# Optimization experiments

Hardware: AMD Instinct MI355X
Metric: run time of the kernel (lower is better)

Reference implementation:

```python
import jax, jax.numpy as jnp
import numpy as np

KR = 3  # kernel_range, SHIFT = 1


def _neighborhood(x):
    """x: [B,H,W,C] -> [B,H,W,9,C] stacking the 3x3 shifted views (zero pad),
    in the same (i,j) raster order as the original loop."""
    B, H, W, C = x.shape
    xp = jnp.pad(x, ((0, 0), (1, 1), (1, 1), (0, 0)))
    views = [xp[:, 1 + i:1 + i + H, 1 + j:1 + j + W, :]
             for i in (-1, 0, 1) for j in (-1, 0, 1)]
    return jnp.stack(views, axis=3)


def _conv(x, w, b):
    # tf.nn.conv2d NHWC, HWIO, SAME, stride 1
    return jax.lax.conv_general_dilated(
        x, w, window_strides=(1, 1), padding='SAME',
        dimension_numbers=('NHWC', 'HWIO', 'NHWC')) + b


def setup_inputs() -> dict:
    key = jax.random.key(0)
    ks = jax.random.split(key, 10)
    B, H, W, D = 8, 128, 128, 64
    g = lambda k, shape, fan: jax.random.normal(k, shape, jnp.float32) * np.float32(1.0 / np.sqrt(fan))
    return {
        'x': jax.random.normal(ks[0], (B, H, W, D), jnp.float32),
        'Q_P': g(ks[1], (D, D), D),
        'K_P': g(ks[2], (D, D), D),
        'V_P': g(ks[3], (D, D), D),
        'ff1_kernel': g(ks[4], (3, 3, D, D), 9 * D),
        'ff1_bias': jax.random.normal(ks[5], (D,), jnp.float32) * 0.01,
        'ff2_kernel': g(ks[6], (3, 3, D, 2 * D), 9 * D),
        'ff2_bias': jax.random.normal(ks[7], (2 * D,), jnp.float32) * 0.01,
        'ff3_kernel': g(ks[8], (3, 3, 2 * D, D), 9 * 2 * D),
        'ff3_bias': jax.random.normal(ks[9], (D,), jnp.float32) * 0.01,
    }


def reference(x, Q_P, K_P, V_P, ff1_kernel, ff1_bias, ff2_kernel, ff2_bias,
              ff3_kernel, ff3_bias):
    B, H, W, D = x.shape
    # 3x3 neighborhood gather (zero padded) and validity mask
    stk = _neighborhood(x)                                   # [B,H,W,9,D]
    mask = _neighborhood(jnp.ones((B, H, W, 1), x.dtype))    # [B,H,W,9,1]
    mask = mask[..., 0]                                      # [B,H,W,9]

    q = jnp.einsum('bhwd,de->bhwe', x, Q_P)                  # [B,H,W,D]
    k = jnp.einsum('bhwkd,de->bhwke', stk, K_P)              # [B,H,W,9,D]
    v = jnp.einsum('bhwkd,de->bhwke', stk, V_P)              # [B,H,W,9,D]

    # NOTE: faithful to original -- scores are MULTIPLIED by the mask
    # (masked entries become 0, not -inf) before softmax over the 9 neighbors.
    scores = jnp.einsum('bhwke,bhwe->bhwk', k, q) * mask     # [B,H,W,9]
    alpha = jax.nn.softmax(scores, axis=-1)
    attn = jnp.einsum('bhwk,bhwke->bhwe', alpha, v)          # [B,H,W,D]

    t = x + attn
    t_in = t
    t = jax.nn.relu(_conv(t, ff1_kernel, ff1_bias))
    t = jax.nn.relu(_conv(t, ff2_kernel, ff2_bias))
    t = jax.nn.relu(_conv(t, ff3_kernel, ff3_bias))
    return t_in + t
```

## Files before the change

### kernel.cpp

```cpp
#include <hip/hip_runtime.h>

typedef unsigned int uint32;
typedef unsigned short u16;
typedef short s16x8 __attribute__((ext_vector_type(8)));
typedef short s16x4 __attribute__((ext_vector_type(4)));
typedef float f32x4 __attribute__((ext_vector_type(4)));

#define DEVINL static __device__ __forceinline__
#define MFMA16(a, b, c) __builtin_amdgcn_mfma_f32_16x16x32_bf16(a, b, c, 0, 0, 0)

DEVINL float bf2f(u16 u){ return __uint_as_float(((uint32)u) << 16); }
DEVINL u16 f2bf(float f){
  uint32 u = __float_as_uint(f);
  u += 0x7fffu + ((u >> 16) & 1u);
  return (u16)(u >> 16);
}
DEVINL uint32 pack2(float a, float b){
  return (uint32)f2bf(a) | (((uint32)f2bf(b)) << 16);
}

__global__ void detect_k(const uint32* __restrict__ x, uint32* __restrict__ flag){
  const int lane = threadIdx.x;
  int sane = 0;
  for (int i = 0; i < 32; ++i){
    uint32 u = x[i * 64 + lane];
    uint32 e = (u >> 7) & 0xffu;
    sane += (e >= 100u && e <= 150u) ? 1 : 0;
  }
  for (int off = 32; off >= 1; off >>= 1) sane += __shfl_xor(sane, off);
  if (lane == 0) *flag = (sane > 1024) ? 1u : 0u;
}

template<int M>
__global__ void cvtall_k(const void* s0, const void* s1, const void* s2,
                         const void* s3, const void* s4, const void* s5,
                         const void* s6, const void* s7, const void* s8,
                         float* __restrict__ wb, const uint32* __restrict__ flag)
{
  if (*flag != (uint32)M) return;
  const int i = blockIdx.x * 256 + threadIdx.x;
  if (i >= 196864) return;
  const void* s; int j;
  if      (i < 4096)   { s = s0; j = i; }
  else if (i < 8192)   { s = s1; j = i - 4096; }
  else if (i < 12288)  { s = s2; j = i - 8192; }
  else if (i < 49152)  { s = s3; j = i - 12288; }
  else if (i < 49216)  { s = s4; j = i - 49152; }
  else if (i < 122944) { s = s5; j = i - 49216; }
  else if (i < 123072) { s = s6; j = i - 122944; }
  else if (i < 196800) { s = s7; j = i - 123072; }
  else                 { s = s8; j = i - 196800; }
  wb[i] = M ? bf2f(((const u16*)s)[j]) : ((const float*)s)[j];
}

__global__ __launch_bounds__(256)
void xcvt_k(const void* __restrict__ x, u16* __restrict__ xb,
            const uint32* __restrict__ flag)
{
  if (*flag != 0u) return;
  const size_t i0 = ((size_t)blockIdx.x * 256 + threadIdx.x) * 8;
  const float4 f0 = ((const float4*)x)[i0 / 4];
  const float4 f1 = ((const float4*)x)[i0 / 4 + 1];
  uint4 o;
  o.x = pack2(f0.x, f0.y); o.y = pack2(f0.z, f0.w);
  o.z = pack2(f1.x, f1.y); o.w = pack2(f1.z, f1.w);
  *(uint4*)(xb + i0) = o;
}

__global__ void gcomp_k(const float* __restrict__ wb, u16* __restrict__ gt){
  const int t = blockIdx.x * 256 + threadIdx.x;
  const int d = t >> 6, c = t & 63;
  const float* __restrict__ K = wb + 4096;
  const float* __restrict__ Q = wb;
  float s = 0.f;
#pragma unroll
  for (int e = 0; e < 64; ++e) s = fmaf(K[d * 64 + e], Q[c * 64 + e], s);
  const u16 hi = f2bf(s);
  gt[t] = hi;
  gt[4096 + t] = f2bf(s - bf2f(hi));
}

__global__ void pack_k(const float* __restrict__ wb, u16* __restrict__ bb){
  int i = blockIdx.x * 256 + threadIdx.x;
  if (i < 4096){
    const int o = i >> 6, c = i & 63;
    bb[8192 + i] = f2bf(wb[8192 + c * 64 + o]);
    return;
  }
  i -= 4096;
  if (i < 4096){
    const int o = i >> 6, c = i & 63;
    const float v = wb[8192 + c * 64 + o];
    bb[12288 + i] = f2bf(v - bf2f(f2bf(v)));
    return;
  }
  i -= 4096;
  if (i < 36864){
    const int chunk = i >> 11, rr = i & 2047, co = rr >> 5, kkp = rr & 31;
    const int slot = (kkp >> 3) ^ ((co >> 1) & 3), kk = slot * 8 + (kkp & 7);
    const int tap = chunk >> 1, ci = (chunk & 1) * 32 + kk;
    bb[16384 + i] = f2bf(wb[12288 + (tap * 64 + ci) * 64 + co]);
    return;
  }
  i -= 36864;
  if (i < 73728){
    const int half = i / 36864, i2 = i - half * 36864;
    const int chunk = i2 >> 11, rr = i2 & 2047, co = rr >> 5, kkp = rr & 31;
    const int slot = (kkp >> 3) ^ ((co >> 1) & 3), kk = slot * 8 + (kkp & 7);
    const int tap = chunk >> 1, ci = (chunk & 1) * 32 + kk;
    bb[53248 + i] = f2bf(wb[49216 + (tap * 64 + ci) * 128 + half * 64 + co]);
    return;
  }
  i -= 73728;
  {
    const int chunk = i >> 11, rr = i & 2047, co = rr >> 5, kkp = rr & 31;
    const int slot = (kkp >> 3) ^ ((co >> 1) & 3), kk = slot * 8 + (kkp & 7);
    const int tap = chunk >> 2, ci = (chunk & 3) * 32 + kk;
    bb[126976 + i] = f2bf(wb[123072 + (tap * 128 + ci) * 64 + co]);
  }
}

template<int ROWS, int CIN, int STRIDE>
DEVINL void stage_tile(const u16* __restrict__ img_base, int h0, int w0, u16* lds){
  constexpr int CH8 = CIN / 8;
  constexpr int NCH = ROWS * 66 * CH8;
  for (int idx = threadIdx.x; idx < NCH; idx += 256){
    const int row  = idx / (66 * CH8);
    const int rem  = idx - row * 66 * CH8;
    const int col  = rem / CH8;
    const int slot = rem - col * CH8;
    const int hi = h0 + row - 1, wi = w0 + col - 1;
    uint4 v = make_uint4(0u, 0u, 0u, 0u);
    if (hi >= 0 && hi < 128 && wi >= 0 && wi < 128)
      v = *(const uint4*)(img_base + (size_t)(hi * 128 + wi) * STRIDE + slot * 8);
    const int dst = (row * 66 + col) * CIN + ((slot ^ (col & 7)) << 3);
    *(uint4*)(lds + dst) = v;
  }
}

template<int COUT_FULL, bool RES, int MOUT>
DEVINL void conv_epilogue(f32x4 acc[4][4], u16* scratch, const u16* __restrict__ res,
                          void* __restrict__ out, int img, int h0, int w0, int co0,
                          int wv, int l15, int lk)
{
  float* tl = (float*)scratch;
  const int lane = threadIdx.x & 63;
#pragma unroll
  for (int pass = 0; pass < 2; ++pass){
    __syncthreads();
#pragma unroll
    for (int at2 = 0; at2 < 2; ++at2){
      const int at = pass * 2 + at2;
      const int pp = wv * 32 + at2 * 16 + lk * 4;
#pragma unroll
      for (int nt = 0; nt < 4; ++nt)
#pragma unroll
        for (int reg = 0; reg < 4; ++reg)
          tl[(pp + reg) * 72 + nt * 16 + l15] = fmaxf(acc[at][nt][reg], 0.f);
    }
    __syncthreads();
    const size_t rowpx = (size_t)img * 16384 + (size_t)(h0 + wv) * 128 + w0 + pass * 32;
    if (MOUT == 0){
#pragma unroll
      for (int k = 0; k < 8; ++k){
        const int px = k * 4 + (lane >> 4);
        const int c4 = (lane & 15) * 4;
        float4 v = *(const float4*)(tl + (wv * 32 + px) * 72 + c4);
        if (RES){
          const uint2 r = *(const uint2*)(res + (rowpx + px) * 64 + c4);
          v.x += bf2f((u16)(r.x & 0xffff)); v.y += bf2f((u16)(r.x >> 16));
          v.z += bf2f((u16)(r.y & 0xffff)); v.w += bf2f((u16)(r.y >> 16));
        }
        *(float4*)((float*)out + (rowpx + px) * 64 + c4) = v;
      }
    } else {
#pragma unroll
      for (int k = 0; k < 4; ++k){
        const int px = k * 8 + (lane >> 3);
        const int c8 = (lane & 7) * 8;
        const float* tp = tl + (wv * 32 + px) * 72 + c8;
        const float4 a = *(const float4*)tp;
        const float4 b = *(const float4*)(tp + 4);
        float v0=a.x, v1=a.y, v2=a.z, v3=a.w, v4=b.x, v5=b.y, v6=b.z, v7=b.w;
        if (RES){
          const uint4 r = *(const uint4*)(res + (rowpx + px) * 64 + c8);
          v0 += bf2f((u16)(r.x & 0xffff)); v1 += bf2f((u16)(r.x >> 16));
          v2 += bf2f((u16)(r.y & 0xffff)); v3 += bf2f((u16)(r.y >> 16));
          v4 += bf2f((u16)(r.z & 0xffff)); v5 += bf2f((u16)(r.z >> 16));
          v6 += bf2f((u16)(r.w & 0xffff)); v7 += bf2f((u16)(r.w >> 16));
        }
        uint4 o;
        o.x = pack2(v0, v1); o.y = pack2(v2, v3);
        o.z = pack2(v4, v5); o.w = pack2(v6, v7);
        *(uint4*)((u16*)out + (rowpx + px) * COUT_FULL + co0 + c8) = o;
      }
    }
  }
}

__global__ __launch_bounds__(256, 4)
void attn_mfma(const u16* __restrict__ xraw, const u16* __restrict__ xcv,
               const u16* __restrict__ gt, const u16* __restrict__ vt,
               u16* __restrict__ tb, const uint32* __restrict__ flag)
{
  __shared__ __align__(16) u16 xh[3 * 66 * 64];
  u16* yl  = xh;
  u16* yl2 = xh + 2 * 66 * 64;
  const int bx0 = blockIdx.x;
  const int bx = (bx0 & 7) * 256 + (bx0 >> 3);
  const int img = bx >> 8, h = (bx >> 1) & 127, w0 = (bx & 1) * 64;
  const int p0 = img * 16384 + h * 128 + w0;
  const u16* __restrict__ xsrc = (*flag != 0u) ? xraw : xcv;
  stage_tile<3, 64, 64>(xsrc + (size_t)img * 16384 * 64, h, w0, xh);
  __syncthreads();

  const int lane = threadIdx.x & 63, wv = threadIdx.x >> 6;
  const int l15 = lane & 15, lk = lane >> 4;
  const int pxm = wv * 16 + l15;

  f32x4 racc[4];
#pragma unroll
  for (int nt = 0; nt < 4; ++nt) racc[nt] = (f32x4){0.f, 0.f, 0.f, 0.f};
#pragma unroll
  for (int half = 0; half < 2; ++half){
#pragma unroll
    for (int ks = 0; ks < 2; ++ks){
      const int colq = pxm + 1;
      const int slot = ks * 4 + lk;
      const s16x8 bx_ = *(const s16x8*)&xh[(66 + colq) * 64 + ((slot ^ (colq & 7)) << 3)];
#pragma unroll
      for (int nt = 0; nt < 4; ++nt){
        const s16x8 ag = *(const s16x8*)(gt + half * 4096 +
                          (size_t)(nt * 16 + l15) * 64 + ks * 32 + lk * 8);
        racc[nt] = MFMA16(ag, bx_, racc[nt]);
      }
    }
  }

  float sc[9];
#pragma unroll
  for (int n = 0; n < 9; ++n){
    const int tr = n / 3, tc = n % 3;
    const int col = pxm + tc;
    const u16* xr = &xh[(tr * 66 + col) * 64];
    float s = 0.f;
#pragma unroll
    for (int nt = 0; nt < 4; ++nt){
      const int slot = nt * 2 + (lk >> 1);
      const s16x4 v = *(const s16x4*)&xr[((slot ^ (col & 7)) << 3) + (lk & 1) * 4];
#pragma unroll
      for (int j = 0; j < 4; ++j)
        s = fmaf(bf2f((u16)v[j]), racc[nt][j], s);
    }
    sc[n] = s;
  }
#pragma unroll
  for (int n = 0; n < 9; ++n){
    sc[n] += __shfl_xor(sc[n], 16);
    sc[n] += __shfl_xor(sc[n], 32);
  }

  float mx = sc[0];
#pragma unroll
  for (int n = 1; n < 9; ++n) mx = fmaxf(mx, sc[n]);
  float sum = 0.f;
#pragma unroll
  for (int n = 0; n < 9; ++n){
    const float e = __expf(sc[n] - mx);
    sc[n] = e; sum += e;
  }
  const float inv = 1.f / sum;
#pragma unroll
  for (int n = 0; n < 9; ++n) sc[n] *= inv;

  float y[16];
#pragma unroll
  for (int j = 0; j < 16; ++j) y[j] = 0.f;
#pragma unroll
  for (int n = 0; n < 9; ++n){
    const int tr = n / 3, tc = n % 3;
    const int col = pxm + tc;
    const u16* xr = &xh[(tr * 66 + col) * 64];
    const float a = sc[n];
#pragma unroll
    for (int sl = 0; sl < 2; ++sl){
      const int slot = lk * 2 + sl;
      const s16x8 v = *(const s16x8*)&xr[(slot ^ (col & 7)) << 3];
#pragma unroll
      for (int j = 0; j < 8; ++j)
        y[sl * 8 + j] = fmaf(a, bf2f((u16)v[j]), y[sl * 8 + j]);
    }
  }

  __syncthreads();

#pragma unroll
  for (int sl = 0; sl < 2; ++sl){
    uint32 hwd[4], lwd[4];
#pragma unroll
    for (int j = 0; j < 4; ++j){
      const float a = y[sl * 8 + 2 * j], b = y[sl * 8 + 2 * j + 1];
      const u16 ha = f2bf(a), hb = f2bf(b);
      hwd[j] = (uint32)ha | ((uint32)hb << 16);
      lwd[j] = (uint32)f2bf(a - bf2f(ha)) | ((uint32)f2bf(b - bf2f(hb)) << 16);
    }
    const int slot = lk * 2 + sl;
    const int off = pxm * 64 + ((slot ^ (pxm & 7)) << 3);
    *(uint4*)&yl [off] = make_uint4(hwd[0], hwd[1], hwd[2], hwd[3]);
    *(uint4*)&yl2[off] = make_uint4(lwd[0], lwd[1], lwd[2], lwd[3]);
  }

  __syncthreads();

  f32x4 tacc[4];
#pragma unroll
  for (int nt = 0; nt < 4; ++nt) tacc[nt] = (f32x4){0.f, 0.f, 0.f, 0.f};
#pragma unroll
  for (int half = 0; half < 2; ++half){
    const u16* yb = half ? yl2 : yl;
#pragma unroll
    for (int ks = 0; ks < 2; ++ks){
      const int px = wv * 16 + l15;
      const int slot = ks * 4 + lk;
      const s16x8 af = *(const s16x8*)&yb[px * 64 + ((slot ^ (px & 7)) << 3)];
#pragma unroll
      for (int nt = 0; nt < 4; ++nt){
        const s16x8 bf = *(const s16x8*)(vt + (size_t)(nt * 16 + l15) * 64 + ks * 32 + lk * 8);
        tacc[nt] = MFMA16(af, bf, tacc[nt]);
      }
    }
  }
#pragma unroll
  for (int nt = 0; nt < 4; ++nt){
#pragma unroll
    for (int reg = 0; reg < 4; ++reg){
      const int pxo = wv * 16 + lk * 4 + reg;
      const int co = nt * 16 + l15;
      const int col = pxo + 1;
      const int elem = (66 + col) * 64 + (((co >> 3) ^ (col & 7)) << 3) + (co & 7);
      tb[(size_t)(p0 + pxo) * 64 + co] = f2bf(bf2f(xh[elem]) + tacc[nt][reg]);
    }
  }
}

template<int COUT_FULL, bool RES, int MOUT>
__global__ __launch_bounds__(256)
void conv_mfma(const u16* __restrict__ in, const u16* __restrict__ wpk,
               const float* __restrict__ bias, const u16* __restrict__ res,
               void* __restrict__ out, const uint32* __restrict__ flag)
{
  if (MOUT >= 0){ if (*flag != (uint32)MOUT) return; }
  __shared__ __align__(16) u16 xh[6 * 66 * 64];

  const int bx0 = blockIdx.x;
  const int bx  = (bx0 & 7) * 64 + (bx0 >> 3);
  const int img = bx >> 6;
  const int rem = bx & 63;
  const int h0  = (rem >> 1) * 4;
  const int w0  = (rem & 1) * 64;
  const int co0 = blockIdx.y * 64;
  const u16* __restrict__ wp = wpk + (size_t)blockIdx.y * 18 * 2048;

  stage_tile<6, 64, 64>(in + (size_t)img * 16384 * 64, h0, w0, xh);
  __syncthreads();

  const int lane = threadIdx.x & 63, wv = threadIdx.x >> 6;
  const int l15 = lane & 15, lk = lane >> 4;

  f32x4 acc[4][4];
#pragma unroll
  for (int nt = 0; nt < 4; ++nt){
    const float b = bias[co0 + nt * 16 + l15];
#pragma unroll
    for (int at = 0; at < 4; ++at) acc[at][nt] = (f32x4){b, b, b, b};
  }

  auto loadB = [&](int ck, s16x8* bb){
#pragma unroll
    for (int nt = 0; nt < 4; ++nt){
      const int co = nt * 16 + l15;
      bb[nt] = *(const s16x8*)(wp + (size_t)ck * 2048 + co * 32 +
                               ((lk ^ ((co >> 1) & 3)) << 3));
    }
  };
  auto doM = [&](int it, s16x8* bb){
    const int tap = it >> 1, ks = it & 1;
    const int tr = tap / 3, tc = tap - tr * 3;
    const int slot = ks * 4 + lk;
    s16x8 av[4];
#pragma unroll
    for (int at = 0; at < 4; ++at){
      const int col = at * 16 + l15 + tc;
      av[at] = *(const s16x8*)&xh[((wv + tr) * 66 + col) * 64 + ((slot ^ (col & 7)) << 3)];
    }
#pragma unroll
    for (int at = 0; at < 4; ++at)
#pragma unroll
      for (int nt = 0; nt < 4; ++nt)
        acc[at][nt] = MFMA16(av[at], bb[nt], acc[at][nt]);
  };

  s16x8 b0[4], b1[4];
  loadB(0, b0);
  loadB(1, b1);
#pragma unroll 1
  for (int it = 0; it < 18; it += 2){
    doM(it, b0);
    if (it + 2 < 18) loadB(it + 2, b0);
    doM(it + 1, b1);
    if (it + 3 < 18) loadB(it + 3, b1);
  }

  conv_epilogue<COUT_FULL, RES, MOUT>(acc, xh, res, out, img, h0, w0, co0, wv, l15, lk);
}

template<int MOUT>
__global__ __launch_bounds__(256)
void conv3_mfma(const u16* __restrict__ in, const u16* __restrict__ wpk,
                const float* __restrict__ bias, const u16* __restrict__ res,
                void* __restrict__ out, const uint32* __restrict__ flag)
{
  if (*flag != (uint32)MOUT) return;
  __shared__ __align__(16) u16 xh[6 * 66 * 64];

  const int bx0 = blockIdx.x;
  const int bx  = (bx0 & 7) * 64 + (bx0 >> 3);
  const int img = bx >> 6;
  const int rem = bx & 63;
  const int h0  = (rem >> 1) * 4;
  const int w0  = (rem & 1) * 64;

  const int lane = threadIdx.x & 63, wv = threadIdx.x >> 6;
  const int l15 = lane & 15, lk = lane >> 4;

  f32x4 acc[4][4];
#pragma unroll
  for (int nt = 0; nt < 4; ++nt){
    const float b = bias[nt * 16 + l15];
#pragma unroll
    for (int at = 0; at < 4; ++at) acc[at][nt] = (f32x4){b, b, b, b};
  }

  auto loadB = [&](int ck, s16x8* bb){
#pragma unroll
    for (int nt = 0; nt < 4; ++nt){
      const int co = nt * 16 + l15;
      bb[nt] = *(const s16x8*)(wpk + (size_t)ck * 2048 + co * 32 +
                               ((lk ^ ((co >> 1) & 3)) << 3));
    }
  };
  auto doM = [&](int it, s16x8* bb){
    const int tap = it >> 1, ks = it & 1;
    const int tr = tap / 3, tc = tap - tr * 3;
    const int slot = ks * 4 + lk;
    s16x8 av[4];
#pragma unroll
    for (int at = 0; at < 4; ++at){
      const int col = at * 16 + l15 + tc;
      av[at] = *(const s16x8*)&xh[((wv + tr) * 66 + col) * 64 + ((slot ^ (col & 7)) << 3)];
    }
#pragma unroll
    for (int at = 0; at < 4; ++at)
#pragma unroll
      for (int nt = 0; nt < 4; ++nt)
        acc[at][nt] = MFMA16(av[at], bb[nt], acc[at][nt]);
  };
  auto chunkOf = [&](int it, int half){
    return ((it >> 1) << 2) + half * 2 + (it & 1);
  };

#pragma unroll 1
  for (int half = 0; half < 2; ++half){
    if (half) __syncthreads();
    stage_tile<6, 64, 128>(in + (size_t)img * 16384 * 128 + half * 64, h0, w0, xh);
    __syncthreads();

    s16x8 b0[4], b1[4];
    loadB(chunkOf(0, half), b0);
    loadB(chunkOf(1, half), b1);
#pragma unroll 1
    for (int it = 0; it < 18; it += 2){
      doM(it, b0);
      if (it + 2 < 18) loadB(chunkOf(it + 2, half), b0);
      doM(it + 1, b1);
      if (it + 3 < 18) loadB(chunkOf(it + 3, half), b1);
    }
  }

  conv_epilogue<64, true, MOUT>(acc, xh, res, out, img, h0, w0, 0, wv, l15, lk);
}

extern "C" void kernel_launch(void* const* d_in, const int* in_sizes, int n_in,
                              void* d_out, int out_size, void* d_ws, size_t ws_size,
                              hipStream_t stream)
{
  (void)in_sizes; (void)n_in; (void)out_size; (void)ws_size;

  char* ws = (char*)d_ws;
  float*  wblob = (float*)ws;
  uint32* flag  = (uint32*)(ws + 983040);
  u16*    bb    = (u16*)(ws + (1u << 20));
  u16*    gt   = bb;
  u16*    vt   = bb + 8192;
  u16*    w1pk = bb + 16384;
  u16*    w2pk = bb + 53248;
  u16*    w3pk = bb + 126976;

  u16*   c2 = (u16*)(ws + (size_t)2097152);
  u16*   tb = (u16*)(ws + (size_t)35651584);
  u16*   xb = (u16*)(ws + (size_t)52428800);
  u16*   c1 = (u16*)(ws + (size_t)52428800);

  detect_k<<<1, 64, 0, stream>>>((const uint32*)d_in[0], flag);

  cvtall_k<0><<<769, 256, 0, stream>>>(d_in[1], d_in[2], d_in[3], d_in[4], d_in[5],
                                       d_in[6], d_in[7], d_in[8], d_in[9], wblob, flag);
  cvtall_k<1><<<769, 256, 0, stream>>>(d_in[1], d_in[2], d_in[3], d_in[4], d_in[5],
                                       d_in[6], d_in[7], d_in[8], d_in[9], wblob, flag);

  xcvt_k<<<4096, 256, 0, stream>>>(d_in[0], xb, flag);

  gcomp_k<<<16, 256, 0, stream>>>(wblob, gt);
  pack_k<<<752, 256, 0, stream>>>(wblob, bb);

  attn_mfma<<<2048, 256, 0, stream>>>((const u16*)d_in[0], xb, gt, vt, tb, flag);

  conv_mfma<64, false, -1><<<dim3(512, 1), 256, 0, stream>>>(
      tb, w1pk, wblob + 49152, nullptr, c1, flag);
  conv_mfma<128, false, -1><<<dim3(512, 2), 256, 0, stream>>>(
      c1, w2pk, wblob + 122944, nullptr, c2, flag);
  conv3_mfma<0><<<512, 256, 0, stream>>>(
      c2, w3pk, wblob + 196800, tb, d_out, flag);
  conv3_mfma<1><<<512, 256, 0, stream>>>(
      c2, w3pk, wblob + 196800, tb, d_out, flag);
}
```

Before: 142.1 us.

## Halve conv tile height to 2 rows and double grid size

The three conv kernels now compute 2-row by 64-column output tiles instead of 4x64. Each of the four waves handles a 32-pixel half row with two M-tiles instead of four. The grid doubles to 1024 blocks and LDS shrinks, and the epilogue is rewritten for the new pixel mapping. The aim is more blocks and higher occupancy across the CUs, at the cost of a larger relative halo (4 staged rows per 2 output rows) and fewer MFMAs per B-fragment load.

```diff
diff --git a/kernel.cpp b/kernel.cpp
--- a/kernel.cpp
+++ b/kernel.cpp
@@ -139,61 +139,61 @@
 }
 
 template<int COUT_FULL, bool RES, int MOUT>
-DEVINL void conv_epilogue(f32x4 acc[4][4], u16* scratch, const u16* __restrict__ res,
-                          void* __restrict__ out, int img, int h0, int w0, int co0,
-                          int wv, int l15, int lk)
+DEVINL void conv_epilogue2(f32x4 acc[2][4], u16* scratch, const u16* __restrict__ res,
+                           void* __restrict__ out, int img, int h0, int w0, int co0,
+                           int wv, int l15, int lk)
 {
   float* tl = (float*)scratch;
   const int lane = threadIdx.x & 63;
-#pragma unroll
-  for (int pass = 0; pass < 2; ++pass){
-    __syncthreads();
-#pragma unroll
-    for (int at2 = 0; at2 < 2; ++at2){
-      const int at = pass * 2 + at2;
-      const int pp = wv * 32 + at2 * 16 + lk * 4;
-#pragma unroll
-      for (int nt = 0; nt < 4; ++nt)
-#pragma unroll
-        for (int reg = 0; reg < 4; ++reg)
-          tl[(pp + reg) * 72 + nt * 16 + l15] = fmaxf(acc[at][nt][reg], 0.f);
-    }
-    __syncthreads();
-    const size_t rowpx = (size_t)img * 16384 + (size_t)(h0 + wv) * 128 + w0 + pass * 32;
-    if (MOUT == 0){
-#pragma unroll
-      for (int k = 0; k < 8; ++k){
-        const int px = k * 4 + (lane >> 4);
-        const int c4 = (lane & 15) * 4;
-        float4 v = *(const float4*)(tl + (wv * 32 + px) * 72 + c4);
-        if (RES){
-          const uint2 r = *(const uint2*)(res + (rowpx + px) * 64 + c4);
-          v.x += bf2f((u16)(r.x & 0xffff)); v.y += bf2f((u16)(r.x >> 16));
-          v.z += bf2f((u16)(r.y & 0xffff)); v.w += bf2f((u16)(r.y >> 16));
-        }
-        *(float4*)((float*)out + (rowpx + px) * 64 + c4) = v;
+  __syncthreads();
+  const int pbase = (wv >> 1) * 64 + (wv & 1) * 32;
+#pragma unroll
+  for (int at = 0; at < 2; ++at)
+#pragma unroll
+    for (int nt = 0; nt < 4; ++nt)
+#pragma unroll
+      for (int reg = 0; reg < 4; ++reg)
+        tl[(pbase + at * 16 + lk * 4 + reg) * 72 + nt * 16 + l15] =
+            fmaxf(acc[at][nt][reg], 0.f);
+  __syncthreads();
+
+  if (MOUT == 0){
+#pragma unroll
+    for (int k = 0; k < 8; ++k){
+      const int pxl = k * 16 + wv * 4 + (lane >> 4);
+      const int c4  = (lane & 15) * 4;
+      const int row = pxl >> 6, col = pxl & 63;
+      const size_t gpx = (size_t)img * 16384 + (size_t)(h0 + row) * 128 + w0 + col;
+      float4 v = *(const float4*)(tl + pxl * 72 + c4);
+      if (RES){
+        const uint2 r = *(const uint2*)(res + gpx * 64 + c4);
+        v.x += bf2f((u16)(r.x & 0xffff)); v.y += bf2f((u16)(r.x >> 16));
+        v.z += bf2f((u16)(r.y & 0xffff)); v.w += bf2f((u16)(r.y >> 16));
       }
-    } else {
-#pragma unroll
-      for (int k = 0; k < 4; ++k){
-        const int px = k * 8 + (lane >> 3);
-        const int c8 = (lane & 7) * 8;
-        const float* tp = tl + (wv * 32 + px) * 72 + c8;
-        const float4 a = *(const float4*)tp;
-        const float4 b = *(const float4*)(tp + 4);
-        float v0=a.x, v1=a.y, v2=a.z, v3=a.w, v4=b.x, v5=b.y, v6=b.z, v7=b.w;
-        if (RES){
-          const uint4 r = *(const uint4*)(res + (rowpx + px) * 64 + c8);
-          v0 += bf2f((u16)(r.x & 0xffff)); v1 += bf2f((u16)(r.x >> 16));
-          v2 += bf2f((u16)(r.y & 0xffff)); v3 += bf2f((u16)(r.y >> 16));
-          v4 += bf2f((u16)(r.z & 0xffff)); v5 += bf2f((u16)(r.z >> 16));
-          v6 += bf2f((u16)(r.w & 0xffff)); v7 += bf2f((u16)(r.w >> 16));
-        }
-        uint4 o;
-        o.x = pack2(v0, v1); o.y = pack2(v2, v3);
-        o.z = pack2(v4, v5); o.w = pack2(v6, v7);
-        *(uint4*)((u16*)out + (rowpx + px) * COUT_FULL + co0 + c8) = o;
+      *(float4*)((float*)out + gpx * 64 + c4) = v;
+    }
+  } else {
+#pragma unroll
+    for (int j = 0; j < 4; ++j){
+      const int pxl = j * 32 + wv * 8 + (lane >> 3);
+      const int c8  = (lane & 7) * 8;
+      const int row = pxl >> 6, col = pxl & 63;
+      const size_t gpx = (size_t)img * 16384 + (size_t)(h0 + row) * 128 + w0 + col;
+      const float* tp = tl + pxl * 72 + c8;
+      const float4 a = *(const float4*)tp;
+      const float4 b = *(const float4*)(tp + 4);
+      float v0=a.x, v1=a.y, v2=a.z, v3=a.w, v4=b.x, v5=b.y, v6=b.z, v7=b.w;
+      if (RES){
+        const uint4 r = *(const uint4*)(res + gpx * 64 + c8);
+        v0 += bf2f((u16)(r.x & 0xffff)); v1 += bf2f((u16)(r.x >> 16));
+        v2 += bf2f((u16)(r.y & 0xffff)); v3 += bf2f((u16)(r.y >> 16));
+        v4 += bf2f((u16)(r.z & 0xffff)); v5 += bf2f((u16)(r.z >> 16));
+        v6 += bf2f((u16)(r.w & 0xffff)); v7 += bf2f((u16)(r.w >> 16));
       }
+      uint4 o;
+      o.x = pack2(v0, v1); o.y = pack2(v2, v3);
+      o.z = pack2(v4, v5); o.w = pack2(v6, v7);
+      *(uint4*)((u16*)out + gpx * COUT_FULL + co0 + c8) = o;
     }
   }
 }
@@ -350,29 +350,30 @@
                void* __restrict__ out, const uint32* __restrict__ flag)
 {
   if (MOUT >= 0){ if (*flag != (uint32)MOUT) return; }
-  __shared__ __align__(16) u16 xh[6 * 66 * 64];
+  __shared__ __align__(16) u16 xh[18432];
 
   const int bx0 = blockIdx.x;
-  const int bx  = (bx0 & 7) * 64 + (bx0 >> 3);
-  const int img = bx >> 6;
-  const int rem = bx & 63;
-  const int h0  = (rem >> 1) * 4;
+  const int bx  = (bx0 & 7) * 128 + (bx0 >> 3);
+  const int img = bx >> 7;
+  const int rem = bx & 127;
+  const int h0  = (rem >> 1) * 2;
   const int w0  = (rem & 1) * 64;
   const int co0 = blockIdx.y * 64;
   const u16* __restrict__ wp = wpk + (size_t)blockIdx.y * 18 * 2048;
 
-  stage_tile<6, 64, 64>(in + (size_t)img * 16384 * 64, h0, w0, xh);
+  stage_tile<4, 64, 64>(in + (size_t)img * 16384 * 64, h0, w0, xh);
   __syncthreads();
 
   const int lane = threadIdx.x & 63, wv = threadIdx.x >> 6;
   const int l15 = lane & 15, lk = lane >> 4;
-
-  f32x4 acc[4][4];
+  const int r   = wv >> 1, c0l = (wv & 1) * 32;
+
+  f32x4 acc[2][4];
 #pragma unroll
   for (int nt = 0; nt < 4; ++nt){
     const float b = bias[co0 + nt * 16 + l15];
 #pragma unroll
-    for (int at = 0; at < 4; ++at) acc[at][nt] = (f32x4){b, b, b, b};
+    for (int at = 0; at < 2; ++at) acc[at][nt] = (f32x4){b, b, b, b};
   }
 
   auto loadB = [&](int ck, s16x8* bb){
@@ -387,14 +388,14 @@
     const int tap = it >> 1, ks = it & 1;
     const int tr = tap / 3, tc = tap - tr * 3;
     const int slot = ks * 4 + lk;
-    s16x8 av[4];
-#pragma unroll
-    for (int at = 0; at < 4; ++at){
-      const int col = at * 16 + l15 + tc;
-      av[at] = *(const s16x8*)&xh[((wv + tr) * 66 + col) * 64 + ((slot ^ (col & 7)) << 3)];
-    }
-#pragma unroll
-    for (int at = 0; at < 4; ++at)
+    s16x8 av[2];
+#pragma unroll
+    for (int at = 0; at < 2; ++at){
+      const int col = c0l + at * 16 + l15 + tc;
+      av[at] = *(const s16x8*)&xh[((r + tr) * 66 + col) * 64 + ((slot ^ (col & 7)) << 3)];
+    }
+#pragma unroll
+    for (int at = 0; at < 2; ++at)
 #pragma unroll
       for (int nt = 0; nt < 4; ++nt)
         acc[at][nt] = MFMA16(av[at], bb[nt], acc[at][nt]);
@@ -411,7 +412,7 @@
     if (it + 3 < 18) loadB(it + 3, b1);
   }
 
-  conv_epilogue<COUT_FULL, RES, MOUT>(acc, xh, res, out, img, h0, w0, co0, wv, l15, lk);
+  conv_epilogue2<COUT_FULL, RES, MOUT>(acc, xh, res, out, img, h0, w0, co0, wv, l15, lk);
 }
 
 template<int MOUT>
@@ -421,24 +422,25 @@
                 void* __restrict__ out, const uint32* __restrict__ flag)
 {
   if (*flag != (uint32)MOUT) return;
-  __shared__ __align__(16) u16 xh[6 * 66 * 64];
+  __shared__ __align__(16) u16 xh[18432];
 
   const int bx0 = blockIdx.x;
-  const int bx  = (bx0 & 7) * 64 + (bx0 >> 3);
-  const int img = bx >> 6;
-  const int rem = bx & 63;
-  const int h0  = (rem >> 1) * 4;
+  const int bx  = (bx0 & 7) * 128 + (bx0 >> 3);
+  const int img = bx >> 7;
+  const int rem = bx & 127;
+  const int h0  = (rem >> 1) * 2;
   const int w0  = (rem & 1) * 64;
 
   const int lane = threadIdx.x & 63, wv = threadIdx.x >> 6;
   const int l15 = lane & 15, lk = lane >> 4;
-
-  f32x4 acc[4][4];
+  const int r   = wv >> 1, c0l = (wv & 1) * 32;
+
+  f32x4 acc[2][4];
 #pragma unroll
   for (int nt = 0; nt < 4; ++nt){
     const float b = bias[nt * 16 + l15];
 #pragma unroll
-    for (int at = 0; at < 4; ++at) acc[at][nt] = (f32x4){b, b, b, b};
+    for (int at = 0; at < 2; ++at) acc[at][nt] = (f32x4){b, b, b, b};
   }
 
   auto loadB = [&](int ck, s16x8* bb){
@@ -453,14 +455,14 @@
     const int tap = it >> 1, ks = it & 1;
     const int tr = tap / 3, tc = tap - tr * 3;
     const int slot = ks * 4 + lk;
-    s16x8 av[4];
-#pragma unroll
-    for (int at = 0; at < 4; ++at){
-      const int col = at * 16 + l15 + tc;
-      av[at] = *(const s16x8*)&xh[((wv + tr) * 66 + col) * 64 + ((slot ^ (col & 7)) << 3)];
-    }
-#pragma unroll
-    for (int at = 0; at < 4; ++at)
+    s16x8 av[2];
+#pragma unroll
+    for (int at = 0; at < 2; ++at){
+      const int col = c0l + at * 16 + l15 + tc;
+      av[at] = *(const s16x8*)&xh[((r + tr) * 66 + col) * 64 + ((slot ^ (col & 7)) << 3)];
+    }
+#pragma unroll
+    for (int at = 0; at < 2; ++at)
 #pragma unroll
       for (int nt = 0; nt < 4; ++nt)
         acc[at][nt] = MFMA16(av[at], bb[nt], acc[at][nt]);
@@ -472,7 +474,7 @@
 #pragma unroll 1
   for (int half = 0; half < 2; ++half){
     if (half) __syncthreads();
-    stage_tile<6, 64, 128>(in + (size_t)img * 16384 * 128 + half * 64, h0, w0, xh);
+    stage_tile<4, 64, 128>(in + (size_t)img * 16384 * 128 + half * 64, h0, w0, xh);
     __syncthreads();
 
     s16x8 b0[4], b1[4];
@@ -487,7 +489,7 @@
     }
   }
 
-  conv_epilogue<64, true, MOUT>(acc, xh, res, out, img, h0, w0, 0, wv, l15, lk);
+  conv_epilogue2<64, true, MOUT>(acc, xh, res, out, img, h0, w0, 0, wv, l15, lk);
 }
 
 extern "C" void kernel_launch(void* const* d_in, const int* in_sizes, int n_in,
@@ -525,12 +527,12 @@
 
   attn_mfma<<<2048, 256, 0, stream>>>((const u16*)d_in[0], xb, gt, vt, tb, flag);
 
-  conv_mfma<64, false, -1><<<dim3(512, 1), 256, 0, stream>>>(
+  conv_mfma<64, false, -1><<<dim3(1024, 1), 256, 0, stream>>>(
       tb, w1pk, wblob + 49152, nullptr, c1, flag);
-  conv_mfma<128, false, -1><<<dim3(512, 2), 256, 0, stream>>>(
+  conv_mfma<128, false, -1><<<dim3(1024, 2), 256, 0, stream>>>(
       c1, w2pk, wblob + 122944, nullptr, c2, flag);
-  conv3_mfma<0><<<512, 256, 0, stream>>>(
+  conv3_mfma<0><<<1024, 256, 0, stream>>>(
       c2, w3pk, wblob + 196800, tb, d_out, flag);
-  conv3_mfma<1><<<512, 256, 0, stream>>>(
+  conv3_mfma<1><<<1024, 256, 0, stream>>>(
       c2, w3pk, wblob + 196800, tb, d_out, flag);
 }
```

New measurement: 138.7 us. -2.4%, faster.
